# Kernel optimization log

Hardware: AMD Instinct MI355X
Metric: run time of the kernel (lower is better)

Reference implementation:

```python
import jax, jax.numpy as jnp
import numpy as np

B, N, D = 1, 4096, 3072
H, DH = 16, 64
INNER = H * DH  # 1024
SCALE = DH ** -0.5
EPS = 1e-5


def setup_inputs() -> dict:
    key = jax.random.key(0)
    ks = jax.random.split(key, 4)
    x = jax.random.normal(ks[0], (B, N, D), jnp.float32)
    pe = jax.random.normal(ks[1], (1, 1, N, DH // 2, 2, 2), jnp.float32)
    w_qkv = jax.random.normal(ks[2], (3 * INNER, D), jnp.float32) * 0.02
    w_out = jax.random.normal(ks[3], (D, INNER), jnp.float32) * 0.02
    ln_g = jnp.ones((D,), jnp.float32)
    ln_b = jnp.zeros((D,), jnp.float32)
    return {"x": x, "pe": pe, "w_qkv": w_qkv, "w_out": w_out, "ln_g": ln_g, "ln_b": ln_b}


def _apply_rope(t, pe):
    # t: [b,h,n,d], pe: [1,1,n,d/2,2,2] (Flux rope layout)
    b, h, n, d = t.shape
    t_ = t.reshape(b, h, n, d // 2, 1, 2)
    out = pe[..., 0] * t_[..., 0] + pe[..., 1] * t_[..., 1]  # [b,h,n,d/2,2]
    return out.reshape(b, h, n, d)


def reference(x, pe, w_qkv, w_out, ln_g, ln_b):
    # LayerNorm (norm2)
    mu = jnp.mean(x, axis=-1, keepdims=True)
    var = jnp.mean((x - mu) ** 2, axis=-1, keepdims=True)
    xn = (x - mu) / jnp.sqrt(var + EPS) * ln_g + ln_b
    # QKV projection (no bias)
    qkv = xn @ w_qkv.T  # [b,n,3*inner]
    q, k, v = jnp.split(qkv, 3, axis=-1)
    def split_heads(t):
        return t.reshape(B, N, H, DH).transpose(0, 2, 1, 3)  # b h n d
    q, k, v = split_heads(q), split_heads(k), split_heads(v)
    # RoPE on q and k (attention_aug_bbox with mask=None, aug idx = -1 -> plain rope attn)
    q = _apply_rope(q, pe)
    k = _apply_rope(k, pe)
    scores = jnp.einsum('bhqd,bhkd->bhqk', q, k) * SCALE
    attn = jax.nn.softmax(scores, axis=-1)
    o = jnp.einsum('bhqk,bhkd->bhqd', attn, v)
    o = o.transpose(0, 2, 1, 3).reshape(B, N, INNER)  # b n (h d)
    return o @ w_out.T  # [b,n,dim]
```

## Files before the change

kernel.cpp:

```cpp
#include <hip/hip_runtime.h>
#include <hip/hip_bf16.h>

typedef unsigned short u16;
typedef __attribute__((ext_vector_type(8))) short bf16x8;
typedef __attribute__((ext_vector_type(4))) float f32x4;

#define N_TOK 4096
#define DMODEL 3072
#define NH 16
#define DHEAD 64
#define INNER 1024
#define SCALE_LOG2E 0.18033688011112042f

__device__ __forceinline__ u16 f2bf(float f) {
    union { float f; unsigned u; } un; un.f = f;
    unsigned r = un.u + 0x7fffu + ((un.u >> 16) & 1u);
    return (u16)(r >> 16);
}
__device__ __forceinline__ float bf2f(u16 u) {
    union { unsigned u; float f; } x; x.u = ((unsigned)u) << 16; return x.f;
}
__device__ __forceinline__ unsigned pk2bf(float a, float b) {
    union { float f; unsigned u; } ua, ub; ua.f = a; ub.f = b;
    return __builtin_amdgcn_perm(ub.u + 0x8000u, ua.u + 0x8000u, 0x07060302u);
}
__device__ __forceinline__ void load_lds16(const u16* g, u16* l) {
    __builtin_amdgcn_global_load_lds(
        (const __attribute__((address_space(1))) unsigned int*)g,
        (__attribute__((address_space(3))) unsigned int*)l, 16, 0, 0);
}

__device__ __forceinline__ bf16x8 build_bp(unsigned u0, unsigned u1,
                                           unsigned w0, unsigned w1) {
    auto a = __builtin_amdgcn_permlane32_swap(u0, w0, false, false);
    auto b = __builtin_amdgcn_permlane16_swap(a[0], a[1], false, false);
    auto c = __builtin_amdgcn_permlane32_swap(u1, w1, false, false);
    auto d = __builtin_amdgcn_permlane16_swap(c[0], c[1], false, false);
    union { unsigned w[4]; bf16x8 v; } r;
    r.w[0] = b[0]; r.w[1] = d[0]; r.w[2] = b[1]; r.w[3] = d[1];
    return r.v;
}

__global__ __launch_bounds__(256) void prep(const float* __restrict__ x,
                                            const float* __restrict__ g,
                                            const float* __restrict__ b,
                                            u16* __restrict__ xn,
                                            const float* __restrict__ w_qkv,
                                            u16* __restrict__ wq,
                                            const float* __restrict__ w_out,
                                            u16* __restrict__ wo) {
    int bid = blockIdx.x;
    int tid = threadIdx.x;
    if (bid < 4096) {
        int row = bid;
        const float4* xr = (const float4*)(x + (size_t)row * DMODEL);
        float4 v[3];
        float s = 0.f, ss = 0.f;
#pragma unroll
        for (int i = 0; i < 3; ++i) {
            v[i] = xr[i * 256 + tid];
            s  += v[i].x + v[i].y + v[i].z + v[i].w;
            ss += v[i].x * v[i].x + v[i].y * v[i].y + v[i].z * v[i].z + v[i].w * v[i].w;
        }
#pragma unroll
        for (int off = 32; off; off >>= 1) {
            s  += __shfl_xor(s, off);
            ss += __shfl_xor(ss, off);
        }
        __shared__ float red[8];
        int wid = tid >> 6, lane = tid & 63;
        if (lane == 0) { red[wid] = s; red[wid + 4] = ss; }
        __syncthreads();
        s  = red[0] + red[1] + red[2] + red[3];
        ss = red[4] + red[5] + red[6] + red[7];
        float mean = s * (1.f / DMODEL);
        float var  = ss * (1.f / DMODEL) - mean * mean;
        float rstd = rsqrtf(var + 1e-5f);
        ushort4* orow = (ushort4*)(xn + (size_t)row * DMODEL);
#pragma unroll
        for (int i = 0; i < 3; ++i) {
            float4 gg = ((const float4*)g)[i * 256 + tid];
            float4 bb = ((const float4*)b)[i * 256 + tid];
            ushort4 o;
            o.x = f2bf((v[i].x - mean) * rstd * gg.x + bb.x);
            o.y = f2bf((v[i].y - mean) * rstd * gg.y + bb.y);
            o.z = f2bf((v[i].z - mean) * rstd * gg.z + bb.z);
            o.w = f2bf((v[i].w - mean) * rstd * gg.w + bb.w);
            orow[i * 256 + tid] = o;
        }
    } else if (bid < 4096 + 2048) {
        const int n4 = 3 * INNER * DMODEL / 4;
        for (int i = (bid - 4096) * 256 + tid; i < n4; i += 2048 * 256) {
            float4 v = ((const float4*)w_qkv)[i];
            ushort4 o;
            o.x = f2bf(v.x); o.y = f2bf(v.y); o.z = f2bf(v.z); o.w = f2bf(v.w);
            ((ushort4*)wq)[i] = o;
        }
    } else {
        const int n4 = DMODEL * INNER / 4;
        for (int i = (bid - 6144) * 256 + tid; i < n4; i += 512 * 256) {
            float4 v = ((const float4*)w_out)[i];
            ushort4 o;
            o.x = f2bf(v.x); o.y = f2bf(v.y); o.z = f2bf(v.z); o.w = f2bf(v.w);
            ((ushort4*)wo)[i] = o;
        }
    }
}


#define VM6 asm volatile("s_waitcnt vmcnt(6)" ::: "memory")
#define VM4 asm volatile("s_waitcnt vmcnt(4)" ::: "memory")
#define VM0 asm volatile("s_waitcnt vmcnt(0)" ::: "memory")
#define LGK8 asm volatile("s_waitcnt lgkmcnt(8)" ::: "memory")
#define NOPS ((void)0)

#define ST_A(d, h, t) do { \
    load_lds16(pA##h##0 + (size_t)(t) * 64, &lds[(d) * 16384 + (h) * 8192 + dq]); \
    load_lds16(pA##h##1 + (size_t)(t) * 64, &lds[(d) * 16384 + (h) * 8192 + dq + 512]); \
  } while (0)
#define ST_B(d, h, t) do { \
    load_lds16(pB##h##0 + (size_t)(t) * 64, &lds[32768 + (d) * 16384 + (h) * 8192 + dq]); \
    load_lds16(pB##h##1 + (size_t)(t) * 64, &lds[32768 + (d) * 16384 + (h) * 8192 + dq + 512]); \
  } while (0)

#define PHASE(d, p, STAGE, PRE, POST) do { \
    bf16x8 afr[2][2]; \
    if ((p) == 0) { \
      _Pragma("unroll") for (int nf = 0; nf < 4; ++nf) { \
        bfr[nf][0] = *(const bf16x8*)&lds[(d) * 16384 + baseB + nf * 1024 + c0]; \
        bfr[nf][1] = *(const bf16x8*)&lds[(d) * 16384 + baseB + nf * 1024 + c1]; \
      } \
    } \
    _Pragma("unroll") for (int mfl = 0; mfl < 2; ++mfl) { \
      afr[mfl][0] = *(const bf16x8*)&lds[(d) * 16384 + (p) * 4096 + mfl * 1024 + baseA + c0]; \
      afr[mfl][1] = *(const bf16x8*)&lds[(d) * 16384 + (p) * 4096 + mfl * 1024 + baseA + c1]; \
    } \
    STAGE; \
    PRE; \
    __builtin_amdgcn_s_barrier(); \
    asm volatile("s_waitcnt lgkmcnt(0)" ::: "memory"); \
    __builtin_amdgcn_sched_barrier(0); \
    __builtin_amdgcn_s_setprio(1); \
    _Pragma("unroll") for (int mfl = 0; mfl < 2; ++mfl) \
      _Pragma("unroll") for (int nf = 0; nf < 4; ++nf) { \
        acc[(p) * 2 + mfl][nf] = __builtin_amdgcn_mfma_f32_16x16x32_bf16(afr[mfl][0], bfr[nf][0], acc[(p) * 2 + mfl][nf], 0, 0, 0); \
        acc[(p) * 2 + mfl][nf] = __builtin_amdgcn_mfma_f32_16x16x32_bf16(afr[mfl][1], bfr[nf][1], acc[(p) * 2 + mfl][nf], 0, 0, 0); \
      } \
    __builtin_amdgcn_s_setprio(0); \
    POST; \
    __builtin_amdgcn_s_barrier(); \
  } while (0)

template <int CBF16>
__global__ __launch_bounds__(512, 2) void gemm256(const u16* __restrict__ A,
                                                  const u16* __restrict__ B,
                                                  void* __restrict__ C,
                                                  int M, int Nn, int K) {
    __shared__ u16 lds[65536];
    const int tid = threadIdx.x;
    const int lane = tid & 63, wid = tid >> 6;
    const int wm = wid >> 2, wn = wid & 3;
    const int l15 = lane & 15, quad = lane >> 4;
    const int sw = l15 & 7;

    int nbx = Nn >> 8;
    int cpx = gridDim.x >> 3;
    int wg = (blockIdx.x & 7) * cpx + (blockIdx.x >> 3);
    int m0 = (wg / nbx) << 8, n0 = (wg % nbx) << 8;

    const int baseA = wm * 2048 + l15 * 64;
    const int baseB = 32768 + wn * 4096 + l15 * 64;
    const int c0 = (quad ^ sw) * 8;
    const int c1 = ((4 + quad) ^ sw) * 8;
    const int dq = wid * 1024;

    const u16 *pA00, *pA01, *pA10, *pA11, *pB00, *pB01, *pB10, *pB11;
    {
        int scol = ((lane & 7) ^ (lane >> 3)) * 8;
#define MKSRC(h, j, PA, PB) { \
        int ell = (h) * 128 + (wid * 2 + (j)) * 8 + (lane >> 3); \
        int g = ell >> 6, wmh = (ell >> 5) & 1, r = ell & 31; \
        PA = A + (size_t)(m0 + wmh * 128 + g * 32 + r) * K + scol; \
        PB = B + (size_t)(n0 + ell) * K + scol; }
        MKSRC(0, 0, pA00, pB00) MKSRC(0, 1, pA01, pB01)
        MKSRC(1, 0, pA10, pB10) MKSRC(1, 1, pA11, pB11)
#undef MKSRC
    }

    f32x4 acc[8][4];
    f32x4 zero4 = {0.f, 0.f, 0.f, 0.f};
#pragma unroll
    for (int i = 0; i < 8; ++i)
#pragma unroll
        for (int j = 0; j < 4; ++j) acc[i][j] = zero4;
    bf16x8 bfr[4][2];

    ST_B(0, 0, 0); ST_B(0, 1, 0); ST_A(0, 0, 0); ST_A(0, 1, 0);
    ST_B(1, 0, 1); ST_B(1, 1, 1); ST_A(1, 0, 1);
    VM6;
    __builtin_amdgcn_s_barrier();

    const int NIT = (K >> 7) - 1;
    for (int i = 0; i < NIT; ++i) {
        int t = 2 * i;
        PHASE(0, 0, ST_A(1, 1, t + 1), LGK8, NOPS);
        PHASE(0, 1, ST_B(0, 0, t + 2), NOPS, NOPS);
        PHASE(0, 2, ST_B(0, 1, t + 2), NOPS, NOPS);
        PHASE(0, 3, ST_A(0, 0, t + 2), NOPS, VM6);
        PHASE(1, 0, ST_A(0, 1, t + 2), LGK8, NOPS);
        PHASE(1, 1, ST_B(1, 0, t + 3), NOPS, NOPS);
        PHASE(1, 2, ST_B(1, 1, t + 3), NOPS, NOPS);
        PHASE(1, 3, ST_A(1, 0, t + 3), NOPS, VM6);
    }
    {
        int T = K >> 6;
        PHASE(0, 0, ST_A(1, 1, T - 1), LGK8, NOPS);
        PHASE(0, 1, NOPS, NOPS, NOPS);
        PHASE(0, 2, NOPS, NOPS, NOPS);
        PHASE(0, 3, NOPS, NOPS, VM0);
        PHASE(1, 0, NOPS, LGK8, NOPS);
        PHASE(1, 1, NOPS, NOPS, NOPS);
        PHASE(1, 2, NOPS, NOPS, NOPS);
        PHASE(1, 3, NOPS, NOPS, NOPS);
    }

#pragma unroll
    for (int mf = 0; mf < 8; ++mf)
#pragma unroll
        for (int nf = 0; nf < 4; ++nf)
#pragma unroll
            for (int r = 0; r < 4; ++r) {
                int rr = m0 + wm * 128 + mf * 16 + quad * 4 + r;
                int cc = n0 + wn * 64 + nf * 16 + l15;
                if (CBF16)
                    ((u16*)C)[(size_t)rr * Nn + cc] = f2bf(acc[mf][nf][r]);
                else
                    ((float*)C)[(size_t)rr * Nn + cc] = acc[mf][nf][r];
            }
}

__global__ __launch_bounds__(256) void rope_vt(const u16* __restrict__ qkv,
                                               const float* __restrict__ pe,
                                               u16* __restrict__ Qr,
                                               u16* __restrict__ Kr,
                                               u16* __restrict__ Vt) {
    int bid = blockIdx.x;
    int tid = threadIdx.x;
    if (bid < 4096) {
        int n = bid;
        const u16* qrow = qkv + (size_t)n * DMODEL;
        const float4* pen = (const float4*)(pe + (size_t)n * 128);
#pragma unroll
        for (int it = 0; it < 2; ++it) {
            int p = it * 256 + tid;
            int h = p >> 5, i = p & 31;
            float4 w = pen[i];
            size_t obase = ((size_t)h * N_TOK + n) * DHEAD + 2 * i;
            unsigned qq = *(const unsigned*)&qrow[h * 64 + 2 * i];
            float q0 = bf2f((u16)qq), q1 = bf2f((u16)(qq >> 16));
            *(unsigned*)&Qr[obase] = pk2bf((w.x * q0 + w.y * q1) * SCALE_LOG2E,
                                           (w.z * q0 + w.w * q1) * SCALE_LOG2E);
            unsigned kk = *(const unsigned*)&qrow[INNER + h * 64 + 2 * i];
            float k0 = bf2f((u16)kk), k1 = bf2f((u16)(kk >> 16));
            *(unsigned*)&Kr[obase] = pk2bf(w.x * k0 + w.y * k1, w.z * k0 + w.w * k1);
        }
    } else {
        __shared__ u16 t[64][65];
        int tb = bid - 4096;
        int n0 = (tb & 63) * 64;
        int h = tb >> 6;
#pragma unroll
        for (int it = 0; it < 4; ++it) {
            int nr = it * 16 + (tid >> 4);
            int dc = (tid & 15) * 4;
            ushort4 v = *(const ushort4*)&qkv[(size_t)(n0 + nr) * DMODEL + 2 * INNER + h * 64 + dc];
            t[dc + 0][nr] = v.x; t[dc + 1][nr] = v.y; t[dc + 2][nr] = v.z; t[dc + 3][nr] = v.w;
        }
        __syncthreads();
#pragma unroll
        for (int it = 0; it < 4; ++it) {
            int dr = it * 16 + (tid >> 4);
            int nc = (tid & 15) * 4;
            ushort4 v;
            v.x = t[dr][nc]; v.y = t[dr][nc + 1]; v.z = t[dr][nc + 2]; v.w = t[dr][nc + 3];
            *(ushort4*)&Vt[((size_t)h * 64 + dr) * N_TOK + n0 + nc] = v;
        }
    }
}


#define FA_STAGE(d, kt) do { \
    load_lds16(&Kh[(size_t)((kt) + rbase + rowoff) * DHEAD + csw], &lds_all[(d) * 8192 + rbase * 64]); \
    load_lds16(&Kh[(size_t)((kt) + rbase + 8 + rowoff) * DHEAD + csw], &lds_all[(d) * 8192 + (rbase + 8) * 64]); \
    load_lds16(&Vh[(size_t)(rbase + rowoff) * N_TOK + (kt) + csw], &lds_all[(d) * 8192 + 4096 + rbase * 64]); \
    load_lds16(&Vh[(size_t)(rbase + 8 + rowoff) * N_TOK + (kt) + csw], &lds_all[(d) * 8192 + 4096 + (rbase + 8) * 64]); \
  } while (0)

#define FA_TILE(d, STAGE_STMT, WAIT_STMT) do { \
    bf16x8 bk[4][2], av[4][2]; \
    _Pragma("unroll") for (int tt = 0; tt < 4; ++tt) \
      _Pragma("unroll") for (int kc = 0; kc < 2; ++kc) { \
        int off = (d) * 8192 + (tt * 16 + l15) * 64 + (((kc * 4 + quad) ^ sw) * 8); \
        bk[tt][kc] = *(const bf16x8*)&lds_all[off]; \
        av[tt][kc] = *(const bf16x8*)&lds_all[off + 4096]; \
      } \
    asm volatile("s_waitcnt lgkmcnt(0)" ::: "memory"); \
    __builtin_amdgcn_sched_barrier(0); \
    __builtin_amdgcn_s_barrier(); \
    __builtin_amdgcn_sched_barrier(0); \
    STAGE_STMT; \
    { \
      f32x4 s[4]; \
      _Pragma("unroll") for (int ntK = 0; ntK < 4; ++ntK) { \
        f32x4 t0 = __builtin_amdgcn_mfma_f32_16x16x32_bf16(bk[ntK][0], aq[0], zero4, 0, 0, 0); \
        s[ntK] = __builtin_amdgcn_mfma_f32_16x16x32_bf16(bk[ntK][1], aq[1], t0, 0, 0, 0); \
      } \
      unsigned pw[4][2]; \
      _Pragma("unroll") for (int ntK = 0; ntK < 4; ++ntK) { \
        pw[ntK][0] = pk2bf(__builtin_amdgcn_exp2f(s[ntK][0]), __builtin_amdgcn_exp2f(s[ntK][1])); \
        pw[ntK][1] = pk2bf(__builtin_amdgcn_exp2f(s[ntK][2]), __builtin_amdgcn_exp2f(s[ntK][3])); \
      } \
      bf16x8 bp0 = build_bp(pw[0][0], pw[0][1], pw[1][0], pw[1][1]); \
      bf16x8 bp1 = build_bp(pw[2][0], pw[2][1], pw[3][0], pw[3][1]); \
      lacc = __builtin_amdgcn_mfma_f32_16x16x32_bf16(ones, bp0, lacc, 0, 0, 0); \
      lacc = __builtin_amdgcn_mfma_f32_16x16x32_bf16(ones, bp1, lacc, 0, 0, 0); \
      _Pragma("unroll") for (int dt = 0; dt < 4; ++dt) { \
        o[dt] = __builtin_amdgcn_mfma_f32_16x16x32_bf16(av[dt][0], bp0, o[dt], 0, 0, 0); \
        o[dt] = __builtin_amdgcn_mfma_f32_16x16x32_bf16(av[dt][1], bp1, o[dt], 0, 0, 0); \
      } \
    } \
    WAIT_STMT; \
    __builtin_amdgcn_s_barrier(); \
    __builtin_amdgcn_sched_barrier(0); \
  } while (0)

__global__ __launch_bounds__(256, 4) void flash_attn(const u16* __restrict__ Q,
                                                     const u16* __restrict__ K,
                                                     const u16* __restrict__ Vt,
                                                     u16* __restrict__ O) {
    __shared__ u16 lds_all[16384];
    int tid = threadIdx.x, lane = tid & 63, wid = tid >> 6;
    int l15 = lane & 15, quad = lane >> 4;
    int sw = l15 & 7;
    int h = blockIdx.y;
    int q0 = blockIdx.x * 64 + wid * 16;
    const u16* Qh = Q + (size_t)h * N_TOK * DHEAD;
    const u16* Kh = K + (size_t)h * N_TOK * DHEAD;
    const u16* Vh = Vt + (size_t)h * DHEAD * N_TOK;

    f32x4 zero4 = {0.f, 0.f, 0.f, 0.f};
    bf16x8 ones;
#pragma unroll
    for (int i = 0; i < 8; ++i) ones[i] = (short)0x3F80;

    bf16x8 aq[2];
#pragma unroll
    for (int kc = 0; kc < 2; ++kc)
        aq[kc] = *(const bf16x8*)&Qh[(size_t)(q0 + l15) * DHEAD + kc * 32 + quad * 8];

    f32x4 o[4], lacc;
#pragma unroll
    for (int dt = 0; dt < 4; ++dt) o[dt] = zero4;
    lacc = zero4;

    int rbase = wid * 16;
    int rowoff = lane >> 3;
    int csw = ((lane & 7) ^ rowoff) * 8;

    FA_STAGE(0, 0);
    FA_STAGE(1, 64);
    VM4;
    __builtin_amdgcn_s_barrier();
    __builtin_amdgcn_sched_barrier(0);

    for (int t = 0; t < 62; t += 2) {
        FA_TILE(0, FA_STAGE(0, (t + 2) * 64), VM4);
        FA_TILE(1, FA_STAGE(1, (t + 3) * 64), VM4);
    }
    FA_TILE(0, NOPS, VM0);
    FA_TILE(1, NOPS, NOPS);

    __syncthreads();
    u16* scratch = lds_all + wid * 1024;
    {
        float rl = 1.f / lacc[0];
#pragma unroll
        for (int dt = 0; dt < 4; ++dt) {
            uint2 ov;
            ov.x = pk2bf(o[dt][0] * rl, o[dt][1] * rl);
            ov.y = pk2bf(o[dt][2] * rl, o[dt][3] * rl);
            *(uint2*)&scratch[l15 * 64 + dt * 16 + quad * 4] = ov;
        }
    }
#pragma unroll
    for (int p = 0; p < 2; ++p) {
        int q_local = p * 8 + (lane >> 3);
        int dcol = (lane & 7) * 8;
        bf16x8 v = *(const bf16x8*)&scratch[q_local * 64 + dcol];
        *(bf16x8*)&O[(size_t)(q0 + q_local) * INNER + h * 64 + dcol] = v;
    }
}

extern "C" void kernel_launch(void* const* d_in, const int* in_sizes, int n_in,
                              void* d_out, int out_size, void* d_ws, size_t ws_size,
                              hipStream_t stream) {
    const float* x     = (const float*)d_in[0];
    const float* pe    = (const float*)d_in[1];
    const float* w_qkv = (const float*)d_in[2];
    const float* w_out = (const float*)d_in[3];
    const float* ln_g  = (const float*)d_in[4];
    const float* ln_b  = (const float*)d_in[5];
    float* out = (float*)d_out;

    char* ws = (char*)d_ws;
    u16* xn  = (u16*)ws;  ws += (size_t)N_TOK * DMODEL * 2;
    u16* wq  = (u16*)ws;  ws += (size_t)3 * INNER * DMODEL * 2;
    u16* wo  = (u16*)ws;  ws += (size_t)DMODEL * INNER * 2;
    u16* qkv = (u16*)ws;  ws += (size_t)N_TOK * DMODEL * 2;
    u16* Qr  = (u16*)ws;  ws += (size_t)NH * N_TOK * DHEAD * 2;
    u16* Kr  = (u16*)ws;  ws += (size_t)NH * N_TOK * DHEAD * 2;
    u16* Vt  = (u16*)ws;  ws += (size_t)NH * DHEAD * N_TOK * 2;
    u16* Ob  = (u16*)ws;  ws += (size_t)N_TOK * INNER * 2;

    prep<<<4096 + 2048 + 512, 256, 0, stream>>>(x, ln_g, ln_b, xn, w_qkv, wq, w_out, wo);
    gemm256<1><<<dim3((N_TOK / 256) * (DMODEL / 256)), 512, 0, stream>>>(xn, wq, qkv, N_TOK, DMODEL, DMODEL);
    rope_vt<<<4096 + 1024, 256, 0, stream>>>(qkv, pe, Qr, Kr, Vt);
    flash_attn<<<dim3(N_TOK / 64, NH), 256, 0, stream>>>(Qr, Kr, Vt, Ob);
    gemm256<0><<<dim3((N_TOK / 256) * (DMODEL / 256)), 512, 0, stream>>>(Ob, wo, out, N_TOK, DMODEL, INNER);
}
```

Baseline: 352.9 us.

## Enlarge flash-attention block to 256 queries with two Q tiles per wave

The flash attention kernel now runs 512 threads per block, 8 waves each handling 32 queries as two 16-row Q tiles. Each K/V tile staged in LDS is therefore reused across four times as many queries, and each thread issues half as many global-to-LDS loads, with the wait counts adjusted to match. The MFMA sections are wrapped in s_setprio to favour matrix work across waves. The cost is more accumulator registers per thread, which may limit occupancy, and only 256 blocks in the grid, which is fewer than before and could underfill the GPU.

```diff
diff --git a/kernel.cpp b/kernel.cpp
--- a/kernel.cpp
+++ b/kernel.cpp
@@ -110,6 +110,7 @@
 
 #define VM6 asm volatile("s_waitcnt vmcnt(6)" ::: "memory")
 #define VM4 asm volatile("s_waitcnt vmcnt(4)" ::: "memory")
+#define VM2 asm volatile("s_waitcnt vmcnt(2)" ::: "memory")
 #define VM0 asm volatile("s_waitcnt vmcnt(0)" ::: "memory")
 #define LGK8 asm volatile("s_waitcnt lgkmcnt(8)" ::: "memory")
 #define NOPS ((void)0)
@@ -290,10 +291,8 @@
 
 
 #define FA_STAGE(d, kt) do { \
-    load_lds16(&Kh[(size_t)((kt) + rbase + rowoff) * DHEAD + csw], &lds_all[(d) * 8192 + rbase * 64]); \
-    load_lds16(&Kh[(size_t)((kt) + rbase + 8 + rowoff) * DHEAD + csw], &lds_all[(d) * 8192 + (rbase + 8) * 64]); \
-    load_lds16(&Vh[(size_t)(rbase + rowoff) * N_TOK + (kt) + csw], &lds_all[(d) * 8192 + 4096 + rbase * 64]); \
-    load_lds16(&Vh[(size_t)(rbase + 8 + rowoff) * N_TOK + (kt) + csw], &lds_all[(d) * 8192 + 4096 + (rbase + 8) * 64]); \
+    load_lds16(&Kh[(size_t)((kt) + krow) * DHEAD + csw], &lds_all[(d) * 8192 + kbase]); \
+    load_lds16(&Vh[(size_t)krow * N_TOK + (kt) + csw], &lds_all[(d) * 8192 + 4096 + kbase]); \
   } while (0)
 
 #define FA_TILE(d, STAGE_STMT, WAIT_STMT) do { \
@@ -309,12 +308,14 @@
     __builtin_amdgcn_s_barrier(); \
     __builtin_amdgcn_sched_barrier(0); \
     STAGE_STMT; \
-    { \
+    _Pragma("unroll") for (int mtQ = 0; mtQ < 2; ++mtQ) { \
       f32x4 s[4]; \
+      __builtin_amdgcn_s_setprio(1); \
       _Pragma("unroll") for (int ntK = 0; ntK < 4; ++ntK) { \
-        f32x4 t0 = __builtin_amdgcn_mfma_f32_16x16x32_bf16(bk[ntK][0], aq[0], zero4, 0, 0, 0); \
-        s[ntK] = __builtin_amdgcn_mfma_f32_16x16x32_bf16(bk[ntK][1], aq[1], t0, 0, 0, 0); \
-      } \
+        f32x4 t0 = __builtin_amdgcn_mfma_f32_16x16x32_bf16(bk[ntK][0], aq[mtQ][0], zero4, 0, 0, 0); \
+        s[ntK] = __builtin_amdgcn_mfma_f32_16x16x32_bf16(bk[ntK][1], aq[mtQ][1], t0, 0, 0, 0); \
+      } \
+      __builtin_amdgcn_s_setprio(0); \
       unsigned pw[4][2]; \
       _Pragma("unroll") for (int ntK = 0; ntK < 4; ++ntK) { \
         pw[ntK][0] = pk2bf(__builtin_amdgcn_exp2f(s[ntK][0]), __builtin_amdgcn_exp2f(s[ntK][1])); \
@@ -322,19 +323,21 @@
       } \
       bf16x8 bp0 = build_bp(pw[0][0], pw[0][1], pw[1][0], pw[1][1]); \
       bf16x8 bp1 = build_bp(pw[2][0], pw[2][1], pw[3][0], pw[3][1]); \
-      lacc = __builtin_amdgcn_mfma_f32_16x16x32_bf16(ones, bp0, lacc, 0, 0, 0); \
-      lacc = __builtin_amdgcn_mfma_f32_16x16x32_bf16(ones, bp1, lacc, 0, 0, 0); \
+      __builtin_amdgcn_s_setprio(1); \
+      lacc[mtQ] = __builtin_amdgcn_mfma_f32_16x16x32_bf16(ones, bp0, lacc[mtQ], 0, 0, 0); \
+      lacc[mtQ] = __builtin_amdgcn_mfma_f32_16x16x32_bf16(ones, bp1, lacc[mtQ], 0, 0, 0); \
       _Pragma("unroll") for (int dt = 0; dt < 4; ++dt) { \
-        o[dt] = __builtin_amdgcn_mfma_f32_16x16x32_bf16(av[dt][0], bp0, o[dt], 0, 0, 0); \
-        o[dt] = __builtin_amdgcn_mfma_f32_16x16x32_bf16(av[dt][1], bp1, o[dt], 0, 0, 0); \
-      } \
+        o[mtQ][dt] = __builtin_amdgcn_mfma_f32_16x16x32_bf16(av[dt][0], bp0, o[mtQ][dt], 0, 0, 0); \
+        o[mtQ][dt] = __builtin_amdgcn_mfma_f32_16x16x32_bf16(av[dt][1], bp1, o[mtQ][dt], 0, 0, 0); \
+      } \
+      __builtin_amdgcn_s_setprio(0); \
     } \
     WAIT_STMT; \
     __builtin_amdgcn_s_barrier(); \
     __builtin_amdgcn_sched_barrier(0); \
   } while (0)
 
-__global__ __launch_bounds__(256, 4) void flash_attn(const u16* __restrict__ Q,
+__global__ __launch_bounds__(512, 4) void flash_attn(const u16* __restrict__ Q,
                                                      const u16* __restrict__ K,
                                                      const u16* __restrict__ Vt,
                                                      u16* __restrict__ O) {
@@ -343,7 +346,7 @@
     int l15 = lane & 15, quad = lane >> 4;
     int sw = l15 & 7;
     int h = blockIdx.y;
-    int q0 = blockIdx.x * 64 + wid * 16;
+    int q0 = blockIdx.x * 256 + wid * 32;
     const u16* Qh = Q + (size_t)h * N_TOK * DHEAD;
     const u16* Kh = K + (size_t)h * N_TOK * DHEAD;
     const u16* Vh = Vt + (size_t)h * DHEAD * N_TOK;
@@ -353,47 +356,54 @@
 #pragma unroll
     for (int i = 0; i < 8; ++i) ones[i] = (short)0x3F80;
 
-    bf16x8 aq[2];
-#pragma unroll
-    for (int kc = 0; kc < 2; ++kc)
-        aq[kc] = *(const bf16x8*)&Qh[(size_t)(q0 + l15) * DHEAD + kc * 32 + quad * 8];
-
-    f32x4 o[4], lacc;
-#pragma unroll
-    for (int dt = 0; dt < 4; ++dt) o[dt] = zero4;
-    lacc = zero4;
-
-    int rbase = wid * 16;
+    bf16x8 aq[2][2];
+#pragma unroll
+    for (int mtQ = 0; mtQ < 2; ++mtQ)
+#pragma unroll
+        for (int kc = 0; kc < 2; ++kc)
+            aq[mtQ][kc] = *(const bf16x8*)&Qh[(size_t)(q0 + mtQ * 16 + l15) * DHEAD + kc * 32 + quad * 8];
+
+    f32x4 o[2][4], lacc[2];
+#pragma unroll
+    for (int mtQ = 0; mtQ < 2; ++mtQ) {
+#pragma unroll
+        for (int dt = 0; dt < 4; ++dt) o[mtQ][dt] = zero4;
+        lacc[mtQ] = zero4;
+    }
+
     int rowoff = lane >> 3;
+    int krow = wid * 8 + rowoff;
+    int kbase = wid * 512;
     int csw = ((lane & 7) ^ rowoff) * 8;
 
     FA_STAGE(0, 0);
     FA_STAGE(1, 64);
-    VM4;
+    VM2;
     __builtin_amdgcn_s_barrier();
     __builtin_amdgcn_sched_barrier(0);
 
     for (int t = 0; t < 62; t += 2) {
-        FA_TILE(0, FA_STAGE(0, (t + 2) * 64), VM4);
-        FA_TILE(1, FA_STAGE(1, (t + 3) * 64), VM4);
+        FA_TILE(0, FA_STAGE(0, (t + 2) * 64), VM2);
+        FA_TILE(1, FA_STAGE(1, (t + 3) * 64), VM2);
     }
     FA_TILE(0, NOPS, VM0);
     FA_TILE(1, NOPS, NOPS);
 
     __syncthreads();
-    u16* scratch = lds_all + wid * 1024;
-    {
-        float rl = 1.f / lacc[0];
+    u16* scratch = lds_all + wid * 2048;
+#pragma unroll
+    for (int mtQ = 0; mtQ < 2; ++mtQ) {
+        float rl = 1.f / lacc[mtQ][0];
 #pragma unroll
         for (int dt = 0; dt < 4; ++dt) {
             uint2 ov;
-            ov.x = pk2bf(o[dt][0] * rl, o[dt][1] * rl);
-            ov.y = pk2bf(o[dt][2] * rl, o[dt][3] * rl);
-            *(uint2*)&scratch[l15 * 64 + dt * 16 + quad * 4] = ov;
-        }
-    }
-#pragma unroll
-    for (int p = 0; p < 2; ++p) {
+            ov.x = pk2bf(o[mtQ][dt][0] * rl, o[mtQ][dt][1] * rl);
+            ov.y = pk2bf(o[mtQ][dt][2] * rl, o[mtQ][dt][3] * rl);
+            *(uint2*)&scratch[(mtQ * 16 + l15) * 64 + dt * 16 + quad * 4] = ov;
+        }
+    }
+#pragma unroll
+    for (int p = 0; p < 4; ++p) {
         int q_local = p * 8 + (lane >> 3);
         int dcol = (lane & 7) * 8;
         bf16x8 v = *(const bf16x8*)&scratch[q_local * 64 + dcol];
@@ -425,6 +435,6 @@
     prep<<<4096 + 2048 + 512, 256, 0, stream>>>(x, ln_g, ln_b, xn, w_qkv, wq, w_out, wo);
     gemm256<1><<<dim3((N_TOK / 256) * (DMODEL / 256)), 512, 0, stream>>>(xn, wq, qkv, N_TOK, DMODEL, DMODEL);
     rope_vt<<<4096 + 1024, 256, 0, stream>>>(qkv, pe, Qr, Kr, Vt);
-    flash_attn<<<dim3(N_TOK / 64, NH), 256, 0, stream>>>(Qr, Kr, Vt, Ob);
+    flash_attn<<<dim3(N_TOK / 256, NH), 512, 0, stream>>>(Qr, Kr, Vt, Ob);
     gemm256<0><<<dim3((N_TOK / 256) * (DMODEL / 256)), 512, 0, stream>>>(Ob, wo, out, N_TOK, DMODEL, INNER);
 }
```

After: 620.4 us. 1.76x slower.
